# Performance work log

Hardware: AMD Instinct MI355X
Metric: run time of the kernel (lower is better)

Reference implementation:

```python
import jax, jax.numpy as jnp
import numpy as np

PAD_IDX = 0
VOCAB = 60
HIDDEN = 128
BATCH = 1024
SEQ = 256


def setup_inputs() -> dict:
    key = jax.random.key(0)
    ks = jax.random.split(key, 6)
    x = jax.random.randint(ks[0], (BATCH, SEQ), 0, VOCAB, dtype=jnp.int64 if jax.config.jax_enable_x64 else jnp.int32)
    lengths = jax.random.randint(ks[1], (BATCH,), 1, SEQ + 1, dtype=x.dtype)
    emb = jax.random.normal(ks[2], (VOCAB, HIDDEN), dtype=jnp.float32) * 0.1
    emb = emb.at[PAD_IDX].set(0.0)  # nn.Embedding padding_idx row is zero
    W_ih = jax.random.normal(ks[3], (HIDDEN, HIDDEN), dtype=jnp.float32) * (1.0 / np.sqrt(HIDDEN))
    W_hh = jax.random.normal(ks[4], (HIDDEN, HIDDEN), dtype=jnp.float32) * (1.0 / np.sqrt(HIDDEN))
    W_fc = jax.random.normal(ks[5], (VOCAB, HIDDEN), dtype=jnp.float32) * (1.0 / np.sqrt(HIDDEN))
    b_fc = jnp.zeros((VOCAB,), dtype=jnp.float32)
    return {"x": x, "lengths": lengths, "emb": emb, "W_ih": W_ih,
            "W_hh": W_hh, "W_fc": W_fc, "b_fc": b_fc}


def reference(x, lengths, emb, W_ih, W_hh, W_fc, b_fc):
    embedded = emb[x]                      # [B, T, H]
    B = embedded.shape[0]
    h0 = jnp.zeros((B, HIDDEN), dtype=embedded.dtype)

    def step(h_prev, x_t):
        # z_t = x_t @ W_ih^T + h_prev @ W_hh^T ; h_t = tanh(z_t)
        h_t = jnp.tanh(x_t @ W_ih.T + h_prev @ W_hh.T)
        return h_t, h_t

    _, hs = jax.lax.scan(step, h0, jnp.swapaxes(embedded, 0, 1))  # hs: [T, B, H]
    outputs = jnp.swapaxes(hs, 0, 1)       # [B, T, H]
    last_out = jnp.take_along_axis(outputs, (lengths - 1)[:, None, None], axis=1)[:, 0, :]  # [B, H]
    return last_out @ W_fc.T + b_fc[None, :]
```

## Files before the change

### kernel.cpp

```cpp
#include <hip/hip_runtime.h>
#include <hip/hip_bf16.h>

#define BATCH 1024
#define SEQ 256
#define HIDDEN 128
#define VOCAB 60
#define MTILE 16
#define ASTRIDE 136
#define XSTRIDE (SEQ + 1)

typedef _Float16 f16x8 __attribute__((ext_vector_type(8)));
typedef _Float16 f16x4 __attribute__((ext_vector_type(4)));
typedef float f32x4 __attribute__((ext_vector_type(4)));

__device__ __forceinline__ float fast_tanh(float x) {
    float e = __builtin_amdgcn_exp2f(x * 2.8853900817779268f);
    return __builtin_fmaf(-2.0f, __builtin_amdgcn_rcpf(e + 1.0f), 1.0f);
}

__global__ void rnn_prep_embw(const float* __restrict__ emb,
                              const float* __restrict__ W_ih,
                              float* __restrict__ embW) {
    const int v = blockIdx.x;
    const int i = threadIdx.x;
    __shared__ __align__(16) float e[HIDDEN];
    e[i] = emb[v * HIDDEN + i];
    __syncthreads();
    const float4* wrow = (const float4*)(W_ih + i * HIDDEN);
    const float4* e4 = (const float4*)e;
    float a0 = 0.f, a1 = 0.f, a2 = 0.f, a3 = 0.f;
#pragma unroll
    for (int j = 0; j < HIDDEN / 4; ++j) {
        float4 w = wrow[j];
        float4 h = e4[j];
        a0 += w.x * h.x; a1 += w.y * h.y; a2 += w.z * h.z; a3 += w.w * h.w;
    }
    embW[v * HIDDEN + i] = (a0 + a1) + (a2 + a3);
}

__global__ void __launch_bounds__(256)
rnn_mfma(const int* __restrict__ x, const int* __restrict__ lengths,
         const float* __restrict__ embW, const float* __restrict__ W_hh,
         const float* __restrict__ W_fc, const float* __restrict__ b_fc,
         float* __restrict__ out) {
    const int tid = threadIdx.x;
    const int wave = tid >> 6;
    const int lane = tid & 63;
    const int q = lane >> 4;
    const int r16 = lane & 15;
    const int c0 = wave * 32;
    const int b0 = blockIdx.x * MTILE;

    __shared__ __align__(16) _Float16 Ah[2][MTILE][ASTRIDE];
    __shared__ __align__(16) _Float16 ew[VOCAB][ASTRIDE];
    __shared__ int xs[MTILE][XSTRIDE];
    __shared__ __align__(16) float hfin[MTILE][HIDDEN];
    __shared__ int lenbuf[MTILE];

    for (int idx = tid; idx < MTILE * SEQ; idx += 256) {
        int r = idx >> 8, t = idx & (SEQ - 1);
        xs[r][t] = x[(b0 + r) * SEQ + t];
    }
    if (tid < MTILE) lenbuf[tid] = lengths[b0 + tid];
    for (int idx = tid; idx < VOCAB * HIDDEN; idx += 256) {
        int v = idx >> 7, c = idx & 127;
        ew[v][c] = (_Float16)embW[idx];
    }
    for (int idx = tid; idx < (int)(sizeof(Ah) / 4); idx += 256)
        ((int*)Ah)[idx] = 0;

    f16x8 Wf[2][4];
#pragma unroll
    for (int nt = 0; nt < 2; ++nt) {
        const float* wrow = W_hh + (c0 + 16 * nt + r16) * HIDDEN + q * 8;
#pragma unroll
        for (int kc = 0; kc < 4; ++kc) {
            const float* p = wrow + kc * 32;
#pragma unroll
            for (int j = 0; j < 8; ++j) Wf[nt][kc][j] = (_Float16)p[j];
        }
    }

    __syncthreads();

    const int mylen = lenbuf[r16];
    int lenmax = 0;
#pragma unroll
    for (int r = 0; r < MTILE; ++r) lenmax = max(lenmax, lenbuf[r]);

    int tok = xs[r16][0];
    f16x4 s0 = *(const f16x4*)&ew[tok][c0 + 4 * q];
    f16x4 s1 = *(const f16x4*)&ew[tok][c0 + 16 + 4 * q];

    int cur = 0;
    f32x4 hout0 = {0.f, 0.f, 0.f, 0.f}, hout1 = {0.f, 0.f, 0.f, 0.f};

    for (int t = 0; t < lenmax; ++t) {
        const _Float16* hb = &Ah[cur][r16][q * 8];
        f16x8 H0 = *(const f16x8*)(hb + 0);
        f16x8 H1 = *(const f16x8*)(hb + 32);
        f16x8 H2 = *(const f16x8*)(hb + 64);
        f16x8 H3 = *(const f16x8*)(hb + 96);

        const int tn = (t + 1 < SEQ) ? t + 1 : SEQ - 1;
        const int tok1 = xs[r16][tn];
        f16x4 sn0 = *(const f16x4*)&ew[tok1][c0 + 4 * q];
        f16x4 sn1 = *(const f16x4*)&ew[tok1][c0 + 16 + 4 * q];

        f32x4 a0 = {(float)s0[0], (float)s0[1], (float)s0[2], (float)s0[3]};
        f32x4 a1 = {(float)s1[0], (float)s1[1], (float)s1[2], (float)s1[3]};
        f32x4 d0 = {0.f, 0.f, 0.f, 0.f}, d1 = {0.f, 0.f, 0.f, 0.f};
        a0 = __builtin_amdgcn_mfma_f32_16x16x32_f16(Wf[0][0], H0, a0, 0, 0, 0);
        a1 = __builtin_amdgcn_mfma_f32_16x16x32_f16(Wf[1][0], H0, a1, 0, 0, 0);
        d0 = __builtin_amdgcn_mfma_f32_16x16x32_f16(Wf[0][2], H2, d0, 0, 0, 0);
        d1 = __builtin_amdgcn_mfma_f32_16x16x32_f16(Wf[1][2], H2, d1, 0, 0, 0);
        a0 = __builtin_amdgcn_mfma_f32_16x16x32_f16(Wf[0][1], H1, a0, 0, 0, 0);
        a1 = __builtin_amdgcn_mfma_f32_16x16x32_f16(Wf[1][1], H1, a1, 0, 0, 0);
        d0 = __builtin_amdgcn_mfma_f32_16x16x32_f16(Wf[0][3], H3, d0, 0, 0, 0);
        d1 = __builtin_amdgcn_mfma_f32_16x16x32_f16(Wf[1][3], H3, d1, 0, 0, 0);
        f32x4 z0 = a0 + d0;
        f32x4 z1 = a1 + d1;

        f32x4 th0, th1;
#pragma unroll
        for (int v = 0; v < 4; ++v) {
            th0[v] = fast_tanh(z0[v]);
            th1[v] = fast_tanh(z1[v]);
        }
        if (t + 1 == mylen) { hout0 = th0; hout1 = th1; }

        uint2 pk0, pk1;
        pk0.x = __builtin_bit_cast(unsigned int, __builtin_amdgcn_cvt_pkrtz(th0[0], th0[1]));
        pk0.y = __builtin_bit_cast(unsigned int, __builtin_amdgcn_cvt_pkrtz(th0[2], th0[3]));
        pk1.x = __builtin_bit_cast(unsigned int, __builtin_amdgcn_cvt_pkrtz(th1[0], th1[1]));
        pk1.y = __builtin_bit_cast(unsigned int, __builtin_amdgcn_cvt_pkrtz(th1[2], th1[3]));

        const int nxt = cur ^ 1;
        *(uint2*)&Ah[nxt][r16][c0 + 4 * q] = pk0;
        *(uint2*)&Ah[nxt][r16][c0 + 16 + 4 * q] = pk1;
        __syncthreads();
        cur = nxt;
        s0 = sn0; s1 = sn1;
    }

#pragma unroll
    for (int v = 0; v < 4; ++v) {
        hfin[r16][c0 + 4 * q + v] = hout0[v];
        hfin[r16][c0 + 16 + 4 * q + v] = hout1[v];
    }
    __syncthreads();

    const int r = tid >> 4;
    const int vbase = tid & 15;
    const float4* hv = (const float4*)hfin[r];
    for (int vo = vbase; vo < VOCAB; vo += 16) {
        const float4* wf = (const float4*)(W_fc + vo * HIDDEN);
        float a0 = 0.f, a1 = 0.f, a2 = 0.f, a3 = 0.f;
#pragma unroll
        for (int j = 0; j < HIDDEN / 4; ++j) {
            float4 a = hv[j];
            float4 w = wf[j];
            a0 += a.x * w.x; a1 += a.y * w.y; a2 += a.z * w.z; a3 += a.w * w.w;
        }
        out[(b0 + r) * VOCAB + vo] = (a0 + a1) + (a2 + a3) + b_fc[vo];
    }
}

extern "C" void kernel_launch(void* const* d_in, const int* in_sizes, int n_in,
                              void* d_out, int out_size, void* d_ws, size_t ws_size,
                              hipStream_t stream) {
    const int* x = (const int*)d_in[0];
    const int* lengths = (const int*)d_in[1];
    const float* emb = (const float*)d_in[2];
    const float* W_ih = (const float*)d_in[3];
    const float* W_hh = (const float*)d_in[4];
    const float* W_fc = (const float*)d_in[5];
    const float* b_fc = (const float*)d_in[6];
    float* out = (float*)d_out;

    float* embW = (float*)d_ws;

    rnn_prep_embw<<<VOCAB, HIDDEN, 0, stream>>>(emb, W_ih, embW);
    rnn_mfma<<<BATCH / MTILE, 256, 0, stream>>>(x, lengths, embW, W_hh, W_fc, b_fc, out);
}
```

Measured before the change: 192.1 us.

## Split hidden columns across eight waves instead of four per batch tile

Doubles the block to 512 threads so each wave owns 16 hidden columns instead of 32. The per-step serial chain drops from 8 MFMAs and 8 tanh per wave to 4 of each, shortening the critical path of every recurrent step. In exchange, the per-step __syncthreads now spans eight waves, which adds barrier cost. The final hidden state is captured from the packed fp16 value rather than the fp32 one, a slight precision change.

Measured after the change: 175.3 us. 1.1x faster.

```diff
diff --git a/kernel.cpp b/kernel.cpp
--- a/kernel.cpp
+++ b/kernel.cpp
@@ -38,7 +38,7 @@
     embW[v * HIDDEN + i] = (a0 + a1) + (a2 + a3);
 }
 
-__global__ void __launch_bounds__(256)
+__global__ void __launch_bounds__(512)
 rnn_mfma(const int* __restrict__ x, const int* __restrict__ lengths,
          const float* __restrict__ embW, const float* __restrict__ W_hh,
          const float* __restrict__ W_fc, const float* __restrict__ b_fc,
@@ -48,7 +48,7 @@
     const int lane = tid & 63;
     const int q = lane >> 4;
     const int r16 = lane & 15;
-    const int c0 = wave * 32;
+    const int c0 = wave * 16;
     const int b0 = blockIdx.x * MTILE;
 
     __shared__ __align__(16) _Float16 Ah[2][MTILE][ASTRIDE];
@@ -57,27 +57,26 @@
     __shared__ __align__(16) float hfin[MTILE][HIDDEN];
     __shared__ int lenbuf[MTILE];
 
-    for (int idx = tid; idx < MTILE * SEQ; idx += 256) {
+    for (int idx = tid; idx < MTILE * SEQ; idx += 512) {
         int r = idx >> 8, t = idx & (SEQ - 1);
         xs[r][t] = x[(b0 + r) * SEQ + t];
     }
     if (tid < MTILE) lenbuf[tid] = lengths[b0 + tid];
-    for (int idx = tid; idx < VOCAB * HIDDEN; idx += 256) {
+    for (int idx = tid; idx < VOCAB * HIDDEN; idx += 512) {
         int v = idx >> 7, c = idx & 127;
         ew[v][c] = (_Float16)embW[idx];
     }
-    for (int idx = tid; idx < (int)(sizeof(Ah) / 4); idx += 256)
+    for (int idx = tid; idx < (int)(sizeof(Ah) / 4); idx += 512)
         ((int*)Ah)[idx] = 0;
 
-    f16x8 Wf[2][4];
-#pragma unroll
-    for (int nt = 0; nt < 2; ++nt) {
-        const float* wrow = W_hh + (c0 + 16 * nt + r16) * HIDDEN + q * 8;
+    f16x8 Wf[4];
+    {
+        const float* wrow = W_hh + (c0 + r16) * HIDDEN + q * 8;
 #pragma unroll
         for (int kc = 0; kc < 4; ++kc) {
             const float* p = wrow + kc * 32;
 #pragma unroll
-            for (int j = 0; j < 8; ++j) Wf[nt][kc][j] = (_Float16)p[j];
+            for (int j = 0; j < 8; ++j) Wf[kc][j] = (_Float16)p[j];
         }
     }
 
@@ -89,11 +88,10 @@
     for (int r = 0; r < MTILE; ++r) lenmax = max(lenmax, lenbuf[r]);
 
     int tok = xs[r16][0];
-    f16x4 s0 = *(const f16x4*)&ew[tok][c0 + 4 * q];
-    f16x4 s1 = *(const f16x4*)&ew[tok][c0 + 16 + 4 * q];
+    f16x4 sd = *(const f16x4*)&ew[tok][c0 + 4 * q];
 
     int cur = 0;
-    f32x4 hout0 = {0.f, 0.f, 0.f, 0.f}, hout1 = {0.f, 0.f, 0.f, 0.f};
+    uint2 cap = {0u, 0u};
 
     for (int t = 0; t < lenmax; ++t) {
         const _Float16* hb = &Ah[cur][r16][q * 8];
@@ -104,56 +102,45 @@
 
         const int tn = (t + 1 < SEQ) ? t + 1 : SEQ - 1;
         const int tok1 = xs[r16][tn];
-        f16x4 sn0 = *(const f16x4*)&ew[tok1][c0 + 4 * q];
-        f16x4 sn1 = *(const f16x4*)&ew[tok1][c0 + 16 + 4 * q];
+        f16x4 sn = *(const f16x4*)&ew[tok1][c0 + 4 * q];
 
-        f32x4 a0 = {(float)s0[0], (float)s0[1], (float)s0[2], (float)s0[3]};
-        f32x4 a1 = {(float)s1[0], (float)s1[1], (float)s1[2], (float)s1[3]};
-        f32x4 d0 = {0.f, 0.f, 0.f, 0.f}, d1 = {0.f, 0.f, 0.f, 0.f};
-        a0 = __builtin_amdgcn_mfma_f32_16x16x32_f16(Wf[0][0], H0, a0, 0, 0, 0);
-        a1 = __builtin_amdgcn_mfma_f32_16x16x32_f16(Wf[1][0], H0, a1, 0, 0, 0);
-        d0 = __builtin_amdgcn_mfma_f32_16x16x32_f16(Wf[0][2], H2, d0, 0, 0, 0);
-        d1 = __builtin_amdgcn_mfma_f32_16x16x32_f16(Wf[1][2], H2, d1, 0, 0, 0);
-        a0 = __builtin_amdgcn_mfma_f32_16x16x32_f16(Wf[0][1], H1, a0, 0, 0, 0);
-        a1 = __builtin_amdgcn_mfma_f32_16x16x32_f16(Wf[1][1], H1, a1, 0, 0, 0);
-        d0 = __builtin_amdgcn_mfma_f32_16x16x32_f16(Wf[0][3], H3, d0, 0, 0, 0);
-        d1 = __builtin_amdgcn_mfma_f32_16x16x32_f16(Wf[1][3], H3, d1, 0, 0, 0);
-        f32x4 z0 = a0 + d0;
-        f32x4 z1 = a1 + d1;
+        f32x4 a = {(float)sd[0], (float)sd[1], (float)sd[2], (float)sd[3]};
+        f32x4 d = {0.f, 0.f, 0.f, 0.f};
+        a = __builtin_amdgcn_mfma_f32_16x16x32_f16(Wf[0], H0, a, 0, 0, 0);
+        d = __builtin_amdgcn_mfma_f32_16x16x32_f16(Wf[2], H2, d, 0, 0, 0);
+        a = __builtin_amdgcn_mfma_f32_16x16x32_f16(Wf[1], H1, a, 0, 0, 0);
+        d = __builtin_amdgcn_mfma_f32_16x16x32_f16(Wf[3], H3, d, 0, 0, 0);
+        f32x4 z = a + d;
 
-        f32x4 th0, th1;
-#pragma unroll
-        for (int v = 0; v < 4; ++v) {
-            th0[v] = fast_tanh(z0[v]);
-            th1[v] = fast_tanh(z1[v]);
-        }
-        if (t + 1 == mylen) { hout0 = th0; hout1 = th1; }
+        float t0 = fast_tanh(z[0]);
+        float t1 = fast_tanh(z[1]);
+        float t2 = fast_tanh(z[2]);
+        float t3 = fast_tanh(z[3]);
 
-        uint2 pk0, pk1;
-        pk0.x = __builtin_bit_cast(unsigned int, __builtin_amdgcn_cvt_pkrtz(th0[0], th0[1]));
-        pk0.y = __builtin_bit_cast(unsigned int, __builtin_amdgcn_cvt_pkrtz(th0[2], th0[3]));
-        pk1.x = __builtin_bit_cast(unsigned int, __builtin_amdgcn_cvt_pkrtz(th1[0], th1[1]));
-        pk1.y = __builtin_bit_cast(unsigned int, __builtin_amdgcn_cvt_pkrtz(th1[2], th1[3]));
+        uint2 pk;
+        pk.x = __builtin_bit_cast(unsigned int, __builtin_amdgcn_cvt_pkrtz(t0, t1));
+        pk.y = __builtin_bit_cast(unsigned int, __builtin_amdgcn_cvt_pkrtz(t2, t3));
+        if (t + 1 == mylen) cap = pk;
 
         const int nxt = cur ^ 1;
-        *(uint2*)&Ah[nxt][r16][c0 + 4 * q] = pk0;
-        *(uint2*)&Ah[nxt][r16][c0 + 16 + 4 * q] = pk1;
+        *(uint2*)&Ah[nxt][r16][c0 + 4 * q] = pk;
         __syncthreads();
         cur = nxt;
-        s0 = sn0; s1 = sn1;
+        sd = sn;
     }
 
+    {
+        f16x4 hc = __builtin_bit_cast(f16x4, cap);
 #pragma unroll
-    for (int v = 0; v < 4; ++v) {
-        hfin[r16][c0 + 4 * q + v] = hout0[v];
-        hfin[r16][c0 + 16 + 4 * q + v] = hout1[v];
+        for (int v = 0; v < 4; ++v)
+            hfin[r16][c0 + 4 * q + v] = (float)hc[v];
     }
     __syncthreads();
 
-    const int r = tid >> 4;
-    const int vbase = tid & 15;
+    const int r = tid >> 5;
+    const int vb = tid & 31;
     const float4* hv = (const float4*)hfin[r];
-    for (int vo = vbase; vo < VOCAB; vo += 16) {
+    for (int vo = vb; vo < VOCAB; vo += 32) {
         const float4* wf = (const float4*)(W_fc + vo * HIDDEN);
         float a0 = 0.f, a1 = 0.f, a2 = 0.f, a3 = 0.f;
 #pragma unroll
@@ -181,5 +168,5 @@
     float* embW = (float*)d_ws;
 
     rnn_prep_embw<<<VOCAB, HIDDEN, 0, stream>>>(emb, W_ih, embW);
-    rnn_mfma<<<BATCH / MTILE, 256, 0, stream>>>(x, lengths, embW, W_hh, W_fc, b_fc, out);
+    rnn_mfma<<<BATCH / MTILE, 512, 0, stream>>>(x, lengths, embW, W_hh, W_fc, b_fc, out);
 }
```

## Process two interleaved batch tiles per block and stream tokens from global

Applied to the files above, without the earlier changes.

Each block now runs two independent 16-row recurrences side by side, sharing the register-resident W_hh fragments and one barrier per step, with their MFMAs interleaved for instruction-level parallelism. Token ids are read straight from global memory two steps ahead instead of being preloaded into shared memory. The grid shrinks to half as many blocks, and per-step work per wave doubles while the serial step count stays the same. This risks a longer per-step critical path on a latency-bound recurrence, and it also leaves more CUs idle.

Result: slower. 294.1 us (+53.1%).

```diff
diff --git a/kernel.cpp b/kernel.cpp
--- a/kernel.cpp
+++ b/kernel.cpp
@@ -6,8 +6,9 @@
 #define HIDDEN 128
 #define VOCAB 60
 #define MTILE 16
+#define NTILES 2
 #define ASTRIDE 136
-#define XSTRIDE (SEQ + 1)
+#define EWSTRIDE 132
 
 typedef _Float16 f16x8 __attribute__((ext_vector_type(8)));
 typedef _Float16 f16x4 __attribute__((ext_vector_type(4)));
@@ -49,23 +50,20 @@
     const int q = lane >> 4;
     const int r16 = lane & 15;
     const int c0 = wave * 32;
-    const int b0 = blockIdx.x * MTILE;
-
-    __shared__ __align__(16) _Float16 Ah[2][MTILE][ASTRIDE];
-    __shared__ __align__(16) _Float16 ew[VOCAB][ASTRIDE];
-    __shared__ int xs[MTILE][XSTRIDE];
-    __shared__ __align__(16) float hfin[MTILE][HIDDEN];
-    __shared__ int lenbuf[MTILE];
-
-    for (int idx = tid; idx < MTILE * SEQ; idx += 256) {
-        int r = idx >> 8, t = idx & (SEQ - 1);
-        xs[r][t] = x[(b0 + r) * SEQ + t];
-    }
-    if (tid < MTILE) lenbuf[tid] = lengths[b0 + tid];
+    const int b0 = blockIdx.x * (NTILES * MTILE);
+    const int rowA = b0 + r16;
+    const int rowB = b0 + MTILE + r16;
+
+    __shared__ __align__(16) _Float16 Ah[2][NTILES][MTILE][ASTRIDE];
+    __shared__ __align__(16) _Float16 ew[VOCAB][EWSTRIDE];
+    __shared__ __align__(16) float hfin[NTILES * MTILE][HIDDEN];
+    __shared__ int lenbuf[NTILES * MTILE];
+
     for (int idx = tid; idx < VOCAB * HIDDEN; idx += 256) {
         int v = idx >> 7, c = idx & 127;
         ew[v][c] = (_Float16)embW[idx];
     }
+    if (tid < NTILES * MTILE) lenbuf[tid] = lengths[b0 + tid];
     for (int idx = tid; idx < (int)(sizeof(Ah) / 4); idx += 256)
         ((int*)Ah)[idx] = 0;
 
@@ -83,77 +81,124 @@
 
     __syncthreads();
 
-    const int mylen = lenbuf[r16];
+    const int mylenA = lenbuf[r16];
+    const int mylenB = lenbuf[MTILE + r16];
     int lenmax = 0;
 #pragma unroll
-    for (int r = 0; r < MTILE; ++r) lenmax = max(lenmax, lenbuf[r]);
-
-    int tok = xs[r16][0];
-    f16x4 s0 = *(const f16x4*)&ew[tok][c0 + 4 * q];
-    f16x4 s1 = *(const f16x4*)&ew[tok][c0 + 16 + 4 * q];
+    for (int r = 0; r < NTILES * MTILE; ++r) lenmax = max(lenmax, lenbuf[r]);
+
+    const int* xrowA = x + rowA * SEQ;
+    const int* xrowB = x + rowB * SEQ;
+    int tokA = xrowA[0], tokB = xrowB[0];
+    f16x4 sA0 = *(const f16x4*)&ew[tokA][c0 + 4 * q];
+    f16x4 sA1 = *(const f16x4*)&ew[tokA][c0 + 16 + 4 * q];
+    f16x4 sB0 = *(const f16x4*)&ew[tokB][c0 + 4 * q];
+    f16x4 sB1 = *(const f16x4*)&ew[tokB][c0 + 16 + 4 * q];
+    int tokA1 = xrowA[1], tokB1 = xrowB[1];
 
     int cur = 0;
-    f32x4 hout0 = {0.f, 0.f, 0.f, 0.f}, hout1 = {0.f, 0.f, 0.f, 0.f};
+    uint2 capA0 = {0u, 0u}, capA1 = {0u, 0u}, capB0 = {0u, 0u}, capB1 = {0u, 0u};
 
     for (int t = 0; t < lenmax; ++t) {
-        const _Float16* hb = &Ah[cur][r16][q * 8];
-        f16x8 H0 = *(const f16x8*)(hb + 0);
-        f16x8 H1 = *(const f16x8*)(hb + 32);
-        f16x8 H2 = *(const f16x8*)(hb + 64);
-        f16x8 H3 = *(const f16x8*)(hb + 96);
-
-        const int tn = (t + 1 < SEQ) ? t + 1 : SEQ - 1;
-        const int tok1 = xs[r16][tn];
-        f16x4 sn0 = *(const f16x4*)&ew[tok1][c0 + 4 * q];
-        f16x4 sn1 = *(const f16x4*)&ew[tok1][c0 + 16 + 4 * q];
-
-        f32x4 a0 = {(float)s0[0], (float)s0[1], (float)s0[2], (float)s0[3]};
-        f32x4 a1 = {(float)s1[0], (float)s1[1], (float)s1[2], (float)s1[3]};
-        f32x4 d0 = {0.f, 0.f, 0.f, 0.f}, d1 = {0.f, 0.f, 0.f, 0.f};
-        a0 = __builtin_amdgcn_mfma_f32_16x16x32_f16(Wf[0][0], H0, a0, 0, 0, 0);
-        a1 = __builtin_amdgcn_mfma_f32_16x16x32_f16(Wf[1][0], H0, a1, 0, 0, 0);
-        d0 = __builtin_amdgcn_mfma_f32_16x16x32_f16(Wf[0][2], H2, d0, 0, 0, 0);
-        d1 = __builtin_amdgcn_mfma_f32_16x16x32_f16(Wf[1][2], H2, d1, 0, 0, 0);
-        a0 = __builtin_amdgcn_mfma_f32_16x16x32_f16(Wf[0][1], H1, a0, 0, 0, 0);
-        a1 = __builtin_amdgcn_mfma_f32_16x16x32_f16(Wf[1][1], H1, a1, 0, 0, 0);
-        d0 = __builtin_amdgcn_mfma_f32_16x16x32_f16(Wf[0][3], H3, d0, 0, 0, 0);
-        d1 = __builtin_amdgcn_mfma_f32_16x16x32_f16(Wf[1][3], H3, d1, 0, 0, 0);
-        f32x4 z0 = a0 + d0;
-        f32x4 z1 = a1 + d1;
-
-        f32x4 th0, th1;
-#pragma unroll
-        for (int v = 0; v < 4; ++v) {
-            th0[v] = fast_tanh(z0[v]);
-            th1[v] = fast_tanh(z1[v]);
-        }
-        if (t + 1 == mylen) { hout0 = th0; hout1 = th1; }
-
-        uint2 pk0, pk1;
-        pk0.x = __builtin_bit_cast(unsigned int, __builtin_amdgcn_cvt_pkrtz(th0[0], th0[1]));
-        pk0.y = __builtin_bit_cast(unsigned int, __builtin_amdgcn_cvt_pkrtz(th0[2], th0[3]));
-        pk1.x = __builtin_bit_cast(unsigned int, __builtin_amdgcn_cvt_pkrtz(th1[0], th1[1]));
-        pk1.y = __builtin_bit_cast(unsigned int, __builtin_amdgcn_cvt_pkrtz(th1[2], th1[3]));
+        const _Float16* hbA = &Ah[cur][0][r16][q * 8];
+        f16x8 HA0 = *(const f16x8*)(hbA + 0);
+        f16x8 HA1 = *(const f16x8*)(hbA + 32);
+        f16x8 HA2 = *(const f16x8*)(hbA + 64);
+        f16x8 HA3 = *(const f16x8*)(hbA + 96);
+        const _Float16* hbB = &Ah[cur][1][r16][q * 8];
+        f16x8 HB0 = *(const f16x8*)(hbB + 0);
+        f16x8 HB1 = *(const f16x8*)(hbB + 32);
+        f16x8 HB2 = *(const f16x8*)(hbB + 64);
+        f16x8 HB3 = *(const f16x8*)(hbB + 96);
+
+        f16x4 snA0 = *(const f16x4*)&ew[tokA1][c0 + 4 * q];
+        f16x4 snA1 = *(const f16x4*)&ew[tokA1][c0 + 16 + 4 * q];
+        f16x4 snB0 = *(const f16x4*)&ew[tokB1][c0 + 4 * q];
+        f16x4 snB1 = *(const f16x4*)&ew[tokB1][c0 + 16 + 4 * q];
+
+        const int t2 = (t + 2 < SEQ) ? t + 2 : SEQ - 1;
+        const int tokA2 = xrowA[t2];
+        const int tokB2 = xrowB[t2];
+
+        f32x4 aA0 = {(float)sA0[0], (float)sA0[1], (float)sA0[2], (float)sA0[3]};
+        f32x4 aA1 = {(float)sA1[0], (float)sA1[1], (float)sA1[2], (float)sA1[3]};
+        f32x4 dA0 = {0.f, 0.f, 0.f, 0.f}, dA1 = {0.f, 0.f, 0.f, 0.f};
+        f32x4 aB0 = {(float)sB0[0], (float)sB0[1], (float)sB0[2], (float)sB0[3]};
+        f32x4 aB1 = {(float)sB1[0], (float)sB1[1], (float)sB1[2], (float)sB1[3]};
+        f32x4 dB0 = {0.f, 0.f, 0.f, 0.f}, dB1 = {0.f, 0.f, 0.f, 0.f};
+
+        aA0 = __builtin_amdgcn_mfma_f32_16x16x32_f16(Wf[0][0], HA0, aA0, 0, 0, 0);
+        aA1 = __builtin_amdgcn_mfma_f32_16x16x32_f16(Wf[1][0], HA0, aA1, 0, 0, 0);
+        aB0 = __builtin_amdgcn_mfma_f32_16x16x32_f16(Wf[0][0], HB0, aB0, 0, 0, 0);
+        aB1 = __builtin_amdgcn_mfma_f32_16x16x32_f16(Wf[1][0], HB0, aB1, 0, 0, 0);
+        dA0 = __builtin_amdgcn_mfma_f32_16x16x32_f16(Wf[0][2], HA2, dA0, 0, 0, 0);
+        dA1 = __builtin_amdgcn_mfma_f32_16x16x32_f16(Wf[1][2], HA2, dA1, 0, 0, 0);
+        dB0 = __builtin_amdgcn_mfma_f32_16x16x32_f16(Wf[0][2], HB2, dB0, 0, 0, 0);
+        dB1 = __builtin_amdgcn_mfma_f32_16x16x32_f16(Wf[1][2], HB2, dB1, 0, 0, 0);
+        aA0 = __builtin_amdgcn_mfma_f32_16x16x32_f16(Wf[0][1], HA1, aA0, 0, 0, 0);
+        aA1 = __builtin_amdgcn_mfma_f32_16x16x32_f16(Wf[1][1], HA1, aA1, 0, 0, 0);
+        aB0 = __builtin_amdgcn_mfma_f32_16x16x32_f16(Wf[0][1], HB1, aB0, 0, 0, 0);
+        aB1 = __builtin_amdgcn_mfma_f32_16x16x32_f16(Wf[1][1], HB1, aB1, 0, 0, 0);
+        dA0 = __builtin_amdgcn_mfma_f32_16x16x32_f16(Wf[0][3], HA3, dA0, 0, 0, 0);
+        dA1 = __builtin_amdgcn_mfma_f32_16x16x32_f16(Wf[1][3], HA3, dA1, 0, 0, 0);
+        dB0 = __builtin_amdgcn_mfma_f32_16x16x32_f16(Wf[0][3], HB3, dB0, 0, 0, 0);
+        dB1 = __builtin_amdgcn_mfma_f32_16x16x32_f16(Wf[1][3], HB3, dB1, 0, 0, 0);
+
+        f32x4 zA0 = aA0 + dA0, zA1 = aA1 + dA1;
+        f32x4 zB0 = aB0 + dB0, zB1 = aB1 + dB1;
 
         const int nxt = cur ^ 1;
-        *(uint2*)&Ah[nxt][r16][c0 + 4 * q] = pk0;
-        *(uint2*)&Ah[nxt][r16][c0 + 16 + 4 * q] = pk1;
+        {
+            float u0 = fast_tanh(zA0[0]), u1 = fast_tanh(zA0[1]);
+            float u2 = fast_tanh(zA0[2]), u3 = fast_tanh(zA0[3]);
+            float v0 = fast_tanh(zA1[0]), v1 = fast_tanh(zA1[1]);
+            float v2 = fast_tanh(zA1[2]), v3 = fast_tanh(zA1[3]);
+            uint2 p0, p1;
+            p0.x = __builtin_bit_cast(unsigned int, __builtin_amdgcn_cvt_pkrtz(u0, u1));
+            p0.y = __builtin_bit_cast(unsigned int, __builtin_amdgcn_cvt_pkrtz(u2, u3));
+            p1.x = __builtin_bit_cast(unsigned int, __builtin_amdgcn_cvt_pkrtz(v0, v1));
+            p1.y = __builtin_bit_cast(unsigned int, __builtin_amdgcn_cvt_pkrtz(v2, v3));
+            if (t + 1 == mylenA) { capA0 = p0; capA1 = p1; }
+            *(uint2*)&Ah[nxt][0][r16][c0 + 4 * q] = p0;
+            *(uint2*)&Ah[nxt][0][r16][c0 + 16 + 4 * q] = p1;
+        }
+        {
+            float u0 = fast_tanh(zB0[0]), u1 = fast_tanh(zB0[1]);
+            float u2 = fast_tanh(zB0[2]), u3 = fast_tanh(zB0[3]);
+            float v0 = fast_tanh(zB1[0]), v1 = fast_tanh(zB1[1]);
+            float v2 = fast_tanh(zB1[2]), v3 = fast_tanh(zB1[3]);
+            uint2 p0, p1;
+            p0.x = __builtin_bit_cast(unsigned int, __builtin_amdgcn_cvt_pkrtz(u0, u1));
+            p0.y = __builtin_bit_cast(unsigned int, __builtin_amdgcn_cvt_pkrtz(u2, u3));
+            p1.x = __builtin_bit_cast(unsigned int, __builtin_amdgcn_cvt_pkrtz(v0, v1));
+            p1.y = __builtin_bit_cast(unsigned int, __builtin_amdgcn_cvt_pkrtz(v2, v3));
+            if (t + 1 == mylenB) { capB0 = p0; capB1 = p1; }
+            *(uint2*)&Ah[nxt][1][r16][c0 + 4 * q] = p0;
+            *(uint2*)&Ah[nxt][1][r16][c0 + 16 + 4 * q] = p1;
+        }
         __syncthreads();
         cur = nxt;
-        s0 = sn0; s1 = sn1;
-    }
-
-#pragma unroll
-    for (int v = 0; v < 4; ++v) {
-        hfin[r16][c0 + 4 * q + v] = hout0[v];
-        hfin[r16][c0 + 16 + 4 * q + v] = hout1[v];
+        sA0 = snA0; sA1 = snA1; sB0 = snB0; sB1 = snB1;
+        tokA1 = tokA2; tokB1 = tokB2;
+    }
+
+    {
+        f16x4 a0 = __builtin_bit_cast(f16x4, capA0), a1 = __builtin_bit_cast(f16x4, capA1);
+        f16x4 b0c = __builtin_bit_cast(f16x4, capB0), b1c = __builtin_bit_cast(f16x4, capB1);
+#pragma unroll
+        for (int v = 0; v < 4; ++v) {
+            hfin[r16][c0 + 4 * q + v] = (float)a0[v];
+            hfin[r16][c0 + 16 + 4 * q + v] = (float)a1[v];
+            hfin[MTILE + r16][c0 + 4 * q + v] = (float)b0c[v];
+            hfin[MTILE + r16][c0 + 16 + 4 * q + v] = (float)b1c[v];
+        }
     }
     __syncthreads();
 
-    const int r = tid >> 4;
-    const int vbase = tid & 15;
+    const int r = tid >> 3;
+    const int vb = tid & 7;
     const float4* hv = (const float4*)hfin[r];
-    for (int vo = vbase; vo < VOCAB; vo += 16) {
+    for (int vo = vb; vo < VOCAB; vo += 8) {
         const float4* wf = (const float4*)(W_fc + vo * HIDDEN);
         float a0 = 0.f, a1 = 0.f, a2 = 0.f, a3 = 0.f;
 #pragma unroll
@@ -181,5 +226,5 @@
     float* embW = (float*)d_ws;
 
     rnn_prep_embw<<<VOCAB, HIDDEN, 0, stream>>>(emb, W_ih, embW);
-    rnn_mfma<<<BATCH / MTILE, 256, 0, stream>>>(x, lengths, embW, W_hh, W_fc, b_fc, out);
-}
+    rnn_mfma<<<BATCH / (NTILES * MTILE), 256, 0, stream>>>(x, lengths, embW, W_hh, W_fc, b_fc, out);
+}
```

## Assign one batch row per block and run only that row's length

Applied to the files above, without the earlier changes.

The RNN kernel now processes a single batch row per workgroup instead of a 16-row tile. This launches 1024 blocks instead of 64, filling many more CUs with 4 blocks per CU via launch bounds. Each block also stops at its own sequence length rather than the tile maximum. In exchange, 15/16 of each MFMA tile computes unused rows, and every block reloads the full embedding-projection table into LDS. The per-step latency chain is unchanged, so the longest row still sets the critical path.

New measurement: 269.7 us. 1.4x slower.

```diff
diff --git a/kernel.cpp b/kernel.cpp
--- a/kernel.cpp
+++ b/kernel.cpp
@@ -5,9 +5,8 @@
 #define SEQ 256
 #define HIDDEN 128
 #define VOCAB 60
-#define MTILE 16
 #define ASTRIDE 136
-#define XSTRIDE (SEQ + 1)
+#define EWSTRIDE 132
 
 typedef _Float16 f16x8 __attribute__((ext_vector_type(8)));
 typedef _Float16 f16x4 __attribute__((ext_vector_type(4)));
@@ -38,7 +37,7 @@
     embW[v * HIDDEN + i] = (a0 + a1) + (a2 + a3);
 }
 
-__global__ void __launch_bounds__(256)
+__global__ void __launch_bounds__(256, 4)
 rnn_mfma(const int* __restrict__ x, const int* __restrict__ lengths,
          const float* __restrict__ embW, const float* __restrict__ W_hh,
          const float* __restrict__ W_fc, const float* __restrict__ b_fc,
@@ -49,25 +48,22 @@
     const int q = lane >> 4;
     const int r16 = lane & 15;
     const int c0 = wave * 32;
-    const int b0 = blockIdx.x * MTILE;
+    const int row = blockIdx.x;
 
-    __shared__ __align__(16) _Float16 Ah[2][MTILE][ASTRIDE];
-    __shared__ __align__(16) _Float16 ew[VOCAB][ASTRIDE];
-    __shared__ int xs[MTILE][XSTRIDE];
-    __shared__ __align__(16) float hfin[MTILE][HIDDEN];
-    __shared__ int lenbuf[MTILE];
+    __shared__ __align__(16) _Float16 Ah[2][ASTRIDE];
+    __shared__ __align__(16) _Float16 ew[VOCAB][EWSTRIDE];
+    __shared__ int xs[SEQ];
+    __shared__ __align__(16) float hfin[HIDDEN];
 
-    for (int idx = tid; idx < MTILE * SEQ; idx += 256) {
-        int r = idx >> 8, t = idx & (SEQ - 1);
-        xs[r][t] = x[(b0 + r) * SEQ + t];
-    }
-    if (tid < MTILE) lenbuf[tid] = lengths[b0 + tid];
     for (int idx = tid; idx < VOCAB * HIDDEN; idx += 256) {
         int v = idx >> 7, c = idx & 127;
         ew[v][c] = (_Float16)embW[idx];
     }
-    for (int idx = tid; idx < (int)(sizeof(Ah) / 4); idx += 256)
-        ((int*)Ah)[idx] = 0;
+    xs[tid] = x[row * SEQ + tid];
+    if (tid < 2 * ASTRIDE / 2) ((int*)Ah)[tid] = 0;
+    if (tid < 16) ((int*)Ah)[256 + tid] = 0;
+
+    const int len = lengths[row];
 
     f16x8 Wf[2][4];
 #pragma unroll
@@ -83,29 +79,25 @@
 
     __syncthreads();
 
-    const int mylen = lenbuf[r16];
-    int lenmax = 0;
-#pragma unroll
-    for (int r = 0; r < MTILE; ++r) lenmax = max(lenmax, lenbuf[r]);
-
-    int tok = xs[r16][0];
+    int tok = xs[0];
     f16x4 s0 = *(const f16x4*)&ew[tok][c0 + 4 * q];
     f16x4 s1 = *(const f16x4*)&ew[tok][c0 + 16 + 4 * q];
+    int tok1 = xs[1];
 
     int cur = 0;
-    f32x4 hout0 = {0.f, 0.f, 0.f, 0.f}, hout1 = {0.f, 0.f, 0.f, 0.f};
+    f32x4 cap0 = {0.f, 0.f, 0.f, 0.f}, cap1 = {0.f, 0.f, 0.f, 0.f};
 
-    for (int t = 0; t < lenmax; ++t) {
-        const _Float16* hb = &Ah[cur][r16][q * 8];
+    for (int t = 0; t < len; ++t) {
+        const _Float16* hb = &Ah[cur][q * 8];
         f16x8 H0 = *(const f16x8*)(hb + 0);
         f16x8 H1 = *(const f16x8*)(hb + 32);
         f16x8 H2 = *(const f16x8*)(hb + 64);
         f16x8 H3 = *(const f16x8*)(hb + 96);
 
-        const int tn = (t + 1 < SEQ) ? t + 1 : SEQ - 1;
-        const int tok1 = xs[r16][tn];
         f16x4 sn0 = *(const f16x4*)&ew[tok1][c0 + 4 * q];
         f16x4 sn1 = *(const f16x4*)&ew[tok1][c0 + 16 + 4 * q];
+        const int t2 = (t + 2 < SEQ) ? t + 2 : SEQ - 1;
+        const int tok2 = xs[t2];
 
         f32x4 a0 = {(float)s0[0], (float)s0[1], (float)s0[2], (float)s0[3]};
         f32x4 a1 = {(float)s1[0], (float)s1[1], (float)s1[2], (float)s1[3]};
@@ -127,42 +119,43 @@
             th0[v] = fast_tanh(z0[v]);
             th1[v] = fast_tanh(z1[v]);
         }
-        if (t + 1 == mylen) { hout0 = th0; hout1 = th1; }
+        if (t + 1 == len) { cap0 = th0; cap1 = th1; }
 
-        uint2 pk0, pk1;
-        pk0.x = __builtin_bit_cast(unsigned int, __builtin_amdgcn_cvt_pkrtz(th0[0], th0[1]));
-        pk0.y = __builtin_bit_cast(unsigned int, __builtin_amdgcn_cvt_pkrtz(th0[2], th0[3]));
-        pk1.x = __builtin_bit_cast(unsigned int, __builtin_amdgcn_cvt_pkrtz(th1[0], th1[1]));
-        pk1.y = __builtin_bit_cast(unsigned int, __builtin_amdgcn_cvt_pkrtz(th1[2], th1[3]));
+        uint2 p0, p1;
+        p0.x = __builtin_bit_cast(unsigned int, __builtin_amdgcn_cvt_pkrtz(th0[0], th0[1]));
+        p0.y = __builtin_bit_cast(unsigned int, __builtin_amdgcn_cvt_pkrtz(th0[2], th0[3]));
+        p1.x = __builtin_bit_cast(unsigned int, __builtin_amdgcn_cvt_pkrtz(th1[0], th1[1]));
+        p1.y = __builtin_bit_cast(unsigned int, __builtin_amdgcn_cvt_pkrtz(th1[2], th1[3]));
 
         const int nxt = cur ^ 1;
-        *(uint2*)&Ah[nxt][r16][c0 + 4 * q] = pk0;
-        *(uint2*)&Ah[nxt][r16][c0 + 16 + 4 * q] = pk1;
+        if (r16 == 0) {
+            *(uint2*)&Ah[nxt][c0 + 4 * q] = p0;
+            *(uint2*)&Ah[nxt][c0 + 16 + 4 * q] = p1;
+        }
         __syncthreads();
         cur = nxt;
         s0 = sn0; s1 = sn1;
+        tok1 = tok2;
     }
 
-#pragma unroll
-    for (int v = 0; v < 4; ++v) {
-        hfin[r16][c0 + 4 * q + v] = hout0[v];
-        hfin[r16][c0 + 16 + 4 * q + v] = hout1[v];
+    if (r16 == 0) {
+        *(f32x4*)&hfin[c0 + 4 * q] = cap0;
+        *(f32x4*)&hfin[c0 + 16 + 4 * q] = cap1;
     }
     __syncthreads();
 
-    const int r = tid >> 4;
-    const int vbase = tid & 15;
-    const float4* hv = (const float4*)hfin[r];
-    for (int vo = vbase; vo < VOCAB; vo += 16) {
-        const float4* wf = (const float4*)(W_fc + vo * HIDDEN);
+    const int c = tid;
+    if (c < VOCAB) {
+        const float4* hv = (const float4*)hfin;
+        const float4* wf = (const float4*)(W_fc + c * HIDDEN);
         float a0 = 0.f, a1 = 0.f, a2 = 0.f, a3 = 0.f;
 #pragma unroll
         for (int j = 0; j < HIDDEN / 4; ++j) {
-            float4 a = hv[j];
+            float4 h = hv[j];
             float4 w = wf[j];
-            a0 += a.x * w.x; a1 += a.y * w.y; a2 += a.z * w.z; a3 += a.w * w.w;
+            a0 += h.x * w.x; a1 += h.y * w.y; a2 += h.z * w.z; a3 += h.w * w.w;
         }
-        out[(b0 + r) * VOCAB + vo] = (a0 + a1) + (a2 + a3) + b_fc[vo];
+        out[row * VOCAB + c] = (a0 + a1) + (a2 + a3) + b_fc[c];
     }
 }
 
@@ -181,5 +174,5 @@
     float* embW = (float*)d_ws;
 
     rnn_prep_embw<<<VOCAB, HIDDEN, 0, stream>>>(emb, W_ih, embW);
-    rnn_mfma<<<BATCH / MTILE, 256, 0, stream>>>(x, lengths, embW, W_hh, W_fc, b_fc, out);
+    rnn_mfma<<<BATCH, 256, 0, stream>>>(x, lengths, embW, W_hh, W_fc, b_fc, out);
 }
```
